# Performance work log

Measured on AMD Instinct MI355X. Metric: run time of the kernel, lower is better.

The kernel has to match this reference:

```python
import jax, jax.numpy as jnp
import numpy as np

B, S, D_MODEL, H = 4, 2048, 1024, 16
HD = D_MODEL // H  # head dim = 64


def setup_inputs() -> dict:
    key = jax.random.key(0)
    k1, k2, k3, k4 = jax.random.split(key, 4)
    x = jax.random.normal(k1, (B, S, D_MODEL), dtype=jnp.float32)
    # weights stored as [d_in, d_out] so projection is x @ W
    scale = 1.0 / np.sqrt(D_MODEL)
    Wq = jax.random.normal(k2, (D_MODEL, D_MODEL), dtype=jnp.float32) * scale
    Wk = jax.random.normal(k3, (D_MODEL, D_MODEL), dtype=jnp.float32) * scale
    Wv = jax.random.normal(k4, (D_MODEL, D_MODEL), dtype=jnp.float32) * scale
    return {"x": x, "Wq": Wq, "Wk": Wk, "Wv": Wv}


def reference(x, Wq, Wk, Wv):
    b, s, d_in = x.shape
    h, hd = H, HD
    # project and split heads -> [b, h, s, hd]
    q = (x @ Wq).reshape(b, s, h, hd).transpose(0, 2, 1, 3)
    k = (x @ Wk).reshape(b, s, h, hd).transpose(0, 2, 1, 3)
    v = (x @ Wv).reshape(b, s, h, hd).transpose(0, 2, 1, 3)
    # raw scores [b, h, s, s]; causal mask (strict upper triangle -> -inf)
    scores = jnp.einsum("bhqd,bhkd->bhqk", q, k)
    causal = jnp.tril(jnp.ones((s, s), dtype=bool))
    scores = jnp.where(causal, scores, -jnp.inf)
    attn = jax.nn.softmax(scores / jnp.sqrt(jnp.float32(hd)), axis=-1)
    ctx = jnp.einsum("bhqk,bhkd->bhqd", attn, v)
    return ctx.transpose(0, 2, 1, 3).reshape(b, s, h * hd)
```

## Files before the change

kernel.cpp:

```cpp
#include <hip/hip_runtime.h>

typedef unsigned short u16;
typedef unsigned int u32;
typedef __bf16 bf16_t;
typedef bf16_t bf16x8 __attribute__((ext_vector_type(8)));
typedef bf16_t bf16x4_t __attribute__((ext_vector_type(4)));
typedef float f32x4 __attribute__((ext_vector_type(4)));
typedef unsigned short ushort8_t __attribute__((ext_vector_type(8)));

#define S_LEN 2048
#define DM 1024
#define NH 16
#define HDIM 64
#define TSTR 136

__device__ __forceinline__ u16 f2b(float f) {
  u32 u = __builtin_bit_cast(u32, f);
  u32 r = (u + 0x7FFFu + ((u >> 16) & 1u)) >> 16;
  return (u16)r;
}

__device__ __forceinline__ void gload16(const void* g, void* l) {
  __builtin_amdgcn_global_load_lds((const __attribute__((address_space(1))) void*)g,
                                   (__attribute__((address_space(3))) void*)l,
                                   16, 0, 0);
}

__device__ __forceinline__ bf16x8 ld_bf8(const u16* p) {
  return *reinterpret_cast<const bf16x8*>(p);
}

__device__ __forceinline__ void stage_rows64(const u16* __restrict__ base, int stride,
                                             u16* __restrict__ dst, int tid, int nchunk) {
#pragma unroll
  for (int i = 0; i < 4; ++i) {
    if (i < nchunk) {
      int ci = i * 256 + tid;
      int row = ci >> 3, col = ci & 7;
      gload16(base + (size_t)row * stride + ((col ^ (row & 7)) << 3), dst + ci * 8);
    }
  }
}
__device__ __forceinline__ void stage_tile256(const u16* __restrict__ base, int stride,
                                              u16* __restrict__ dst, int tid) {
  stage_rows64(base, stride, dst, tid, 2);
}
__device__ __forceinline__ bf16x8 ld_swz64(const u16* lds, int row, int chunk) {
  return ld_bf8(lds + row * 64 + ((chunk ^ (row & 7)) << 3));
}

__global__ __launch_bounds__(256) void k_cvt(const float* __restrict__ in, u16* __restrict__ out) {
  int i = (blockIdx.x * 256 + threadIdx.x) * 4;
  float4 v = *reinterpret_cast<const float4*>(in + i);
  ushort4 o = make_ushort4(f2b(v.x), f2b(v.y), f2b(v.z), f2b(v.w));
  *reinterpret_cast<ushort4*>(out + i) = o;
}

__global__ __launch_bounds__(256) void k_wt3(const float* __restrict__ Wq, const float* __restrict__ Wk,
                                             const float* __restrict__ Wv, u16* __restrict__ Wt) {
  __shared__ float t[32][33];
  const float* W = (blockIdx.z == 0) ? Wq : (blockIdx.z == 1) ? Wk : Wv;
  u16* dst = Wt + (size_t)blockIdx.z * (DM * DM);
  int n0 = blockIdx.x * 32, k0 = blockIdx.y * 32;
  int tx = threadIdx.x & 31, ty = threadIdx.x >> 5;
#pragma unroll
  for (int i = 0; i < 32; i += 8)
    t[ty + i][tx] = W[(size_t)(k0 + ty + i) * DM + n0 + tx];
  __syncthreads();
#pragma unroll
  for (int i = 0; i < 32; i += 8)
    dst[(size_t)(n0 + ty + i) * DM + k0 + tx] = f2b(t[tx][ty + i]);
}

template <bool TRANSPOSED>
__device__ __forceinline__ void gemm_loop(const u16* __restrict__ Ag, const u16* __restrict__ Bg,
                                          u16* __restrict__ At, u16* __restrict__ Bt,
                                          f32x4 (&acc)[4][4], int tid, int l15, int lg,
                                          int wm, int wn) {
  for (int kt = 0; kt < 16; ++kt) {
    int kk = kt * 64;
    stage_rows64(Ag + kk, DM, At, tid, 4);
    stage_rows64(Bg + kk, DM, Bt, tid, 4);
    __syncthreads();
#pragma unroll
    for (int ks = 0; ks < 2; ++ks) {
      bf16x8 af[4], bfr[4];
#pragma unroll
      for (int mi = 0; mi < 4; ++mi)
        af[mi] = ld_swz64(At, wm * 64 + mi * 16 + l15, ks * 4 + lg);
#pragma unroll
      for (int ni = 0; ni < 4; ++ni)
        bfr[ni] = ld_swz64(Bt, wn * 64 + ni * 16 + l15, ks * 4 + lg);
#pragma unroll
      for (int mi = 0; mi < 4; ++mi)
#pragma unroll
        for (int ni = 0; ni < 4; ++ni) {
          if (TRANSPOSED)
            acc[mi][ni] = __builtin_amdgcn_mfma_f32_16x16x32_bf16(bfr[ni], af[mi], acc[mi][ni], 0, 0, 0);
          else
            acc[mi][ni] = __builtin_amdgcn_mfma_f32_16x16x32_bf16(af[mi], bfr[ni], acc[mi][ni], 0, 0, 0);
        }
    }
    __syncthreads();
  }
}

__global__ __launch_bounds__(256, 3) void k_gemm(const u16* __restrict__ Xb, const u16* __restrict__ Wt_all,
                                                 u16* __restrict__ Out_all, u16* __restrict__ Vt,
                                                 float qscale) {
  __shared__ __attribute__((aligned(16))) u16 smem[128 * TSTR];
  u16* At = smem;
  u16* Bt = smem + 8192;
  int bx = blockIdx.x, by = blockIdx.y;
  int n0g = bx * 128, m0 = by * 128;
  int which = n0g >> 10;
  int n0 = n0g & 1023;
  int tid = threadIdx.x;
  int lane = tid & 63, w = tid >> 6;
  int l15 = lane & 15, lg = lane >> 4;
  int wm = w >> 1, wn = w & 1;

  const u16* Ag = Xb + (size_t)m0 * DM;
  const u16* Bg = Wt_all + (size_t)n0g * DM;

  f32x4 acc[4][4] = {};
  u16* T = smem;
  int b = m0 >> 11, s0 = m0 & 2047;
  int base_h = n0 >> 6;

  if (which < 2) {
    gemm_loop<true>(Ag, Bg, At, Bt, acc, tid, l15, lg, wm, wn);
    float scale = (which == 0) ? qscale : 1.0f;
    u16* Out = Out_all + (size_t)which * (size_t)(4 * NH * S_LEN * HDIM);
#pragma unroll
    for (int mi = 0; mi < 4; ++mi) {
#pragma unroll
      for (int ni = 0; ni < 4; ++ni) {
        ushort4 w4 = make_ushort4(f2b(acc[mi][ni][0] * scale), f2b(acc[mi][ni][1] * scale),
                                  f2b(acc[mi][ni][2] * scale), f2b(acc[mi][ni][3] * scale));
        *reinterpret_cast<ushort4*>(T + (wm * 64 + mi * 16 + l15) * TSTR +
                                    wn * 64 + ni * 16 + lg * 4) = w4;
      }
    }
    __syncthreads();
#pragma unroll
    for (int pass = 0; pass < 8; ++pass) {
      int row = pass * 16 + (tid >> 4);
      int col = (tid & 15) * 8;
      ushort8_t v = *reinterpret_cast<const ushort8_t*>(T + row * TSTR + col);
      int h = base_h + (col >> 6), hd = col & 63;
      *reinterpret_cast<ushort8_t*>(Out + ((size_t)(b * NH + h) * S_LEN + s0 + row) * HDIM + hd) = v;
    }
  } else {
    gemm_loop<false>(Ag, Bg, At, Bt, acc, tid, l15, lg, wm, wn);
#pragma unroll
    for (int mi = 0; mi < 4; ++mi) {
#pragma unroll
      for (int ni = 0; ni < 4; ++ni) {
        ushort4 w4 = make_ushort4(f2b(acc[mi][ni][0]), f2b(acc[mi][ni][1]),
                                  f2b(acc[mi][ni][2]), f2b(acc[mi][ni][3]));
        *reinterpret_cast<ushort4*>(T + (wn * 64 + ni * 16 + l15) * TSTR +
                                    wm * 64 + mi * 16 + lg * 4) = w4;
      }
    }
    __syncthreads();
#pragma unroll
    for (int pass = 0; pass < 8; ++pass) {
      int row = pass * 16 + (tid >> 4);
      int col = (tid & 15) * 8;
      ushort8_t v = *reinterpret_cast<const ushort8_t*>(T + row * TSTR + col);
      int h = base_h + (row >> 6), hd = row & 63;
      *reinterpret_cast<ushort8_t*>(Vt + ((size_t)((b * NH + h) * HDIM + hd)) * S_LEN + s0 + col) = v;
    }
  }
}

__device__ __forceinline__ void attn_strip(const u16* __restrict__ Qp, const u16* __restrict__ Kp,
                                           const u16* __restrict__ Vp, float* __restrict__ out,
                                           int b, int h, int qbase, int w, int tid, int lane, int nt,
                                           u16 (*Kd)[64 * 64], u16 (*Vd)[64 * 64],
                                           u16* __restrict__ Pw) {
  int l15 = lane & 15, lg = lane >> 4;
  int qrow = qbase + w * 16;
  bf16x8 qf0 = ld_bf8(Qp + (size_t)(qrow + l15) * HDIM + lg * 8);
  bf16x8 qf1 = ld_bf8(Qp + (size_t)(qrow + l15) * HDIM + 32 + lg * 8);
  f32x4 o[4] = {};
  float ls = 0.f;
  int qa = qrow + l15;
  int psw = (l15 & 7) << 3;

  stage_tile256(Kp, HDIM, Kd[0], tid);
  stage_tile256(Vp, S_LEN, Vd[0], tid);

  for (int kt = 0; kt < nt; ++kt) {
    int k0 = kt * 64;
    int cur = kt & 1;
    asm volatile("s_waitcnt vmcnt(0)" ::: "memory");
    __builtin_amdgcn_sched_barrier(0);
    __builtin_amdgcn_s_barrier();
    __builtin_amdgcn_sched_barrier(0);
    if (kt + 1 < nt) {
      stage_tile256(Kp + (size_t)(k0 + 64) * HDIM, HDIM, Kd[cur ^ 1], tid);
      stage_tile256(Vp + k0 + 64, S_LEN, Vd[cur ^ 1], tid);
    }

    f32x4 sc[4];
    __builtin_amdgcn_s_setprio(1);
#pragma unroll
    for (int kb = 0; kb < 4; ++kb) {
      bf16x8 kf0 = ld_swz64(Kd[cur], kb * 16 + l15, lg);
      bf16x8 kf1 = ld_swz64(Kd[cur], kb * 16 + l15, 4 + lg);
      f32x4 z = {};
      z = __builtin_amdgcn_mfma_f32_16x16x32_bf16(kf0, qf0, z, 0, 0, 0);
      sc[kb] = __builtin_amdgcn_mfma_f32_16x16x32_bf16(kf1, qf1, sc[kb] = z, 0, 0, 0);
    }
    __builtin_amdgcn_s_setprio(0);

    if (kt == nt - 1) {
#pragma unroll
      for (int kb = 0; kb < 4; ++kb) {
        bf16x4_t pw;
#pragma unroll
        for (int r = 0; r < 4; ++r) {
          int key = k0 + kb * 16 + lg * 4 + r;
          float e = __builtin_amdgcn_exp2f(sc[kb][r]);
          e = (key > qa) ? 0.f : e;
          ls += e;
          pw[r] = (bf16_t)e;
        }
        *reinterpret_cast<bf16x4_t*>(Pw + l15 * 64 + ((kb * 16 + lg * 4) ^ psw)) = pw;
      }
    } else {
#pragma unroll
      for (int kb = 0; kb < 4; ++kb) {
        bf16x4_t pw;
#pragma unroll
        for (int r = 0; r < 4; ++r) {
          float e = __builtin_amdgcn_exp2f(sc[kb][r]);
          ls += e;
          pw[r] = (bf16_t)e;
        }
        *reinterpret_cast<bf16x4_t*>(Pw + l15 * 64 + ((kb * 16 + lg * 4) ^ psw)) = pw;
      }
    }
    asm volatile("" ::: "memory");
    bf16x8 pf0 = ld_bf8(Pw + l15 * 64 + ((lg * 8) ^ psw));
    bf16x8 pf1 = ld_bf8(Pw + l15 * 64 + ((32 + lg * 8) ^ psw));

    __builtin_amdgcn_s_setprio(1);
#pragma unroll
    for (int n = 0; n < 4; ++n) {
      bf16x8 vf0 = ld_swz64(Vd[cur], n * 16 + l15, lg);
      bf16x8 vf1 = ld_swz64(Vd[cur], n * 16 + l15, 4 + lg);
      o[n] = __builtin_amdgcn_mfma_f32_16x16x32_bf16(pf0, vf0, o[n], 0, 0, 0);
      o[n] = __builtin_amdgcn_mfma_f32_16x16x32_bf16(pf1, vf1, o[n], 0, 0, 0);
    }
    __builtin_amdgcn_s_setprio(0);
  }

  ls += __shfl_xor(ls, 16);
  ls += __shfl_xor(ls, 32);
  float l0 = __shfl(ls, lg * 4 + 0);
  float l1 = __shfl(ls, lg * 4 + 1);
  float l2 = __shfl(ls, lg * 4 + 2);
  float l3 = __shfl(ls, lg * 4 + 3);
  float lsr[4] = {l0, l1, l2, l3};
#pragma unroll
  for (int r = 0; r < 4; ++r) {
    float inv = 1.f / lsr[r];
    int row = qrow + lg * 4 + r;
#pragma unroll
    for (int n = 0; n < 4; ++n)
      out[((size_t)b * S_LEN + row) * DM + h * HDIM + n * 16 + l15] = o[n][r] * inv;
  }
}

__global__ __launch_bounds__(256, 4) void k_attn(const u16* __restrict__ Qb, const u16* __restrict__ Kb,
                                                 const u16* __restrict__ Vtb, float* __restrict__ out) {
  __shared__ u16 Kd[2][64 * 64];
  __shared__ u16 Vd[2][64 * 64];
  __shared__ u16 Plds[4][16 * 64];
  int j = blockIdx.x;
  int m = j >> 3;
  int x = m & 15;
  int bh = (j & 7) + 8 * (m >> 4);
  int tid = threadIdx.x, lane = tid & 63, w = tid >> 6;
  int b = bh >> 4, h = bh & 15;
  const u16* Qp = Qb + (size_t)bh * S_LEN * HDIM;
  const u16* Kp = Kb + (size_t)bh * S_LEN * HDIM;
  const u16* Vp = Vtb + (size_t)bh * HDIM * S_LEN;
  u16* Pw = Plds[w];
  attn_strip(Qp, Kp, Vp, out, b, h, x * 64, w, tid, lane, x + 1, Kd, Vd, Pw);
  attn_strip(Qp, Kp, Vp, out, b, h, (31 - x) * 64, w, tid, lane, 32 - x, Kd, Vd, Pw);
}

extern "C" void kernel_launch(void* const* d_in, const int* in_sizes, int n_in,
                              void* d_out, int out_size, void* d_ws, size_t ws_size,
                              hipStream_t stream) {
  const float* x  = (const float*)d_in[0];
  const float* Wq = (const float*)d_in[1];
  const float* Wk = (const float*)d_in[2];
  const float* Wv = (const float*)d_in[3];
  float* out = (float*)d_out;

  u16* ws  = (u16*)d_ws;
  u16* xb  = ws;
  u16* wqt = xb + 8388608;
  u16* Qb  = wqt + 3145728;
  u16* Kb  = Qb + 8388608;
  u16* Vtb = Kb + 8388608;

  const float qscale = 0.125f * 1.44269504088896f;

  k_cvt<<<8192, 256, 0, stream>>>(x, xb);
  k_wt3<<<dim3(32, 32, 3), 256, 0, stream>>>(Wq, Wk, Wv, wqt);
  k_gemm<<<dim3(24, 64), 256, 0, stream>>>(xb, wqt, Qb, Vtb, qscale);
  k_attn<<<1024, 256, 0, stream>>>(Qb, Kb, Vtb, out);
}
```

Baseline: 126.9 us.

## Fuse paired causal strips into one K/V sweep sharing staged tiles

The two query strips a block handles (x and 31-x) used to make separate passes over K/V. They now share one loop over the longer strip's key tiles, and the short strip is processed on the same staged tiles while kt <= x. This halves the global-to-LDS K/V staging and removes the second prologue and pipeline ramp. Block-to-x mapping is also reversed for odd groups of 256 to vary scheduling. The cost is more live registers (two sets of Q fragments and accumulators) under launch_bounds(256,4), which risks spills or lower occupancy.

```diff
diff --git a/kernel.cpp b/kernel.cpp
--- a/kernel.cpp
+++ b/kernel.cpp
@@ -175,19 +175,111 @@
   }
 }
 
-__device__ __forceinline__ void attn_strip(const u16* __restrict__ Qp, const u16* __restrict__ Kp,
-                                           const u16* __restrict__ Vp, float* __restrict__ out,
-                                           int b, int h, int qbase, int w, int tid, int lane, int nt,
-                                           u16 (*Kd)[64 * 64], u16 (*Vd)[64 * 64],
-                                           u16* __restrict__ Pw) {
+__device__ __forceinline__ void strip_tile(bool diag, int k0, int qa,
+                                           const u16* __restrict__ Kt, const u16* __restrict__ Vt,
+                                           u16* __restrict__ Pw, int l15, int lg, int psw,
+                                           bf16x8 qf0, bf16x8 qf1, f32x4 (&o)[4], float& ls) {
+  f32x4 sc[4];
+  __builtin_amdgcn_s_setprio(1);
+#pragma unroll
+  for (int kb = 0; kb < 4; ++kb) {
+    bf16x8 kf0 = ld_swz64(Kt, kb * 16 + l15, lg);
+    bf16x8 kf1 = ld_swz64(Kt, kb * 16 + l15, 4 + lg);
+    f32x4 z = {};
+    z = __builtin_amdgcn_mfma_f32_16x16x32_bf16(kf0, qf0, z, 0, 0, 0);
+    sc[kb] = __builtin_amdgcn_mfma_f32_16x16x32_bf16(kf1, qf1, sc[kb] = z, 0, 0, 0);
+  }
+  __builtin_amdgcn_s_setprio(0);
+
+  if (diag) {
+#pragma unroll
+    for (int kb = 0; kb < 4; ++kb) {
+      bf16x4_t pw;
+#pragma unroll
+      for (int r = 0; r < 4; ++r) {
+        int key = k0 + kb * 16 + lg * 4 + r;
+        float e = __builtin_amdgcn_exp2f(sc[kb][r]);
+        e = (key > qa) ? 0.f : e;
+        ls += e;
+        pw[r] = (bf16_t)e;
+      }
+      *reinterpret_cast<bf16x4_t*>(Pw + l15 * 64 + ((kb * 16 + lg * 4) ^ psw)) = pw;
+    }
+  } else {
+#pragma unroll
+    for (int kb = 0; kb < 4; ++kb) {
+      bf16x4_t pw;
+#pragma unroll
+      for (int r = 0; r < 4; ++r) {
+        float e = __builtin_amdgcn_exp2f(sc[kb][r]);
+        ls += e;
+        pw[r] = (bf16_t)e;
+      }
+      *reinterpret_cast<bf16x4_t*>(Pw + l15 * 64 + ((kb * 16 + lg * 4) ^ psw)) = pw;
+    }
+  }
+  asm volatile("" ::: "memory");
+  bf16x8 pf0 = ld_bf8(Pw + l15 * 64 + ((lg * 8) ^ psw));
+  bf16x8 pf1 = ld_bf8(Pw + l15 * 64 + ((32 + lg * 8) ^ psw));
+
+  __builtin_amdgcn_s_setprio(1);
+#pragma unroll
+  for (int n = 0; n < 4; ++n) {
+    bf16x8 vf0 = ld_swz64(Vt, n * 16 + l15, lg);
+    bf16x8 vf1 = ld_swz64(Vt, n * 16 + l15, 4 + lg);
+    o[n] = __builtin_amdgcn_mfma_f32_16x16x32_bf16(pf0, vf0, o[n], 0, 0, 0);
+    o[n] = __builtin_amdgcn_mfma_f32_16x16x32_bf16(pf1, vf1, o[n], 0, 0, 0);
+  }
+  __builtin_amdgcn_s_setprio(0);
+}
+
+__device__ __forceinline__ void strip_out(float* __restrict__ out, int b, int h, int qrow,
+                                          int l15, int lg, f32x4 (&o)[4], float ls) {
+  ls += __shfl_xor(ls, 16);
+  ls += __shfl_xor(ls, 32);
+  float lsr[4];
+#pragma unroll
+  for (int r = 0; r < 4; ++r) lsr[r] = __shfl(ls, lg * 4 + r);
+#pragma unroll
+  for (int r = 0; r < 4; ++r) {
+    float inv = 1.f / lsr[r];
+    int row = qrow + lg * 4 + r;
+#pragma unroll
+    for (int n = 0; n < 4; ++n)
+      out[((size_t)b * S_LEN + row) * DM + h * HDIM + n * 16 + l15] = o[n][r] * inv;
+  }
+}
+
+__global__ __launch_bounds__(256, 4) void k_attn(const u16* __restrict__ Qb, const u16* __restrict__ Kb,
+                                                 const u16* __restrict__ Vtb, float* __restrict__ out) {
+  __shared__ u16 Kd[2][64 * 64];
+  __shared__ u16 Vd[2][64 * 64];
+  __shared__ u16 Plds[4][16 * 64];
+  int j = blockIdx.x;
+  int m = j >> 3;
+  int xr = m & 15;
+  int x = ((j >> 8) & 1) ? (15 - xr) : xr;
+  int bh = (j & 7) + 8 * (m >> 4);
+  int tid = threadIdx.x, lane = tid & 63, w = tid >> 6;
+  int b = bh >> 4, h = bh & 15;
   int l15 = lane & 15, lg = lane >> 4;
-  int qrow = qbase + w * 16;
-  bf16x8 qf0 = ld_bf8(Qp + (size_t)(qrow + l15) * HDIM + lg * 8);
-  bf16x8 qf1 = ld_bf8(Qp + (size_t)(qrow + l15) * HDIM + 32 + lg * 8);
-  f32x4 o[4] = {};
-  float ls = 0.f;
-  int qa = qrow + l15;
   int psw = (l15 & 7) << 3;
+  const u16* Qp = Qb + (size_t)bh * S_LEN * HDIM;
+  const u16* Kp = Kb + (size_t)bh * S_LEN * HDIM;
+  const u16* Vp = Vtb + (size_t)bh * HDIM * S_LEN;
+  u16* Pw = Plds[w];
+
+  int qrowA = x * 64 + w * 16;
+  int qrowB = (31 - x) * 64 + w * 16;
+  int qaA = qrowA + l15, qaB = qrowB + l15;
+  bf16x8 qfA0 = ld_bf8(Qp + (size_t)(qrowA + l15) * HDIM + lg * 8);
+  bf16x8 qfA1 = ld_bf8(Qp + (size_t)(qrowA + l15) * HDIM + 32 + lg * 8);
+  bf16x8 qfB0 = ld_bf8(Qp + (size_t)(qrowB + l15) * HDIM + lg * 8);
+  bf16x8 qfB1 = ld_bf8(Qp + (size_t)(qrowB + l15) * HDIM + 32 + lg * 8);
+  f32x4 oA[4] = {}, oB[4] = {};
+  float lsA = 0.f, lsB = 0.f;
+
+  int nt = 32 - x;
 
   stage_tile256(Kp, HDIM, Kd[0], tid);
   stage_tile256(Vp, S_LEN, Vd[0], tid);
@@ -203,95 +295,13 @@
       stage_tile256(Kp + (size_t)(k0 + 64) * HDIM, HDIM, Kd[cur ^ 1], tid);
       stage_tile256(Vp + k0 + 64, S_LEN, Vd[cur ^ 1], tid);
     }
-
-    f32x4 sc[4];
-    __builtin_amdgcn_s_setprio(1);
-#pragma unroll
-    for (int kb = 0; kb < 4; ++kb) {
-      bf16x8 kf0 = ld_swz64(Kd[cur], kb * 16 + l15, lg);
-      bf16x8 kf1 = ld_swz64(Kd[cur], kb * 16 + l15, 4 + lg);
-      f32x4 z = {};
-      z = __builtin_amdgcn_mfma_f32_16x16x32_bf16(kf0, qf0, z, 0, 0, 0);
-      sc[kb] = __builtin_amdgcn_mfma_f32_16x16x32_bf16(kf1, qf1, sc[kb] = z, 0, 0, 0);
-    }
-    __builtin_amdgcn_s_setprio(0);
-
-    if (kt == nt - 1) {
-#pragma unroll
-      for (int kb = 0; kb < 4; ++kb) {
-        bf16x4_t pw;
-#pragma unroll
-        for (int r = 0; r < 4; ++r) {
-          int key = k0 + kb * 16 + lg * 4 + r;
-          float e = __builtin_amdgcn_exp2f(sc[kb][r]);
-          e = (key > qa) ? 0.f : e;
-          ls += e;
-          pw[r] = (bf16_t)e;
-        }
-        *reinterpret_cast<bf16x4_t*>(Pw + l15 * 64 + ((kb * 16 + lg * 4) ^ psw)) = pw;
-      }
-    } else {
-#pragma unroll
-      for (int kb = 0; kb < 4; ++kb) {
-        bf16x4_t pw;
-#pragma unroll
-        for (int r = 0; r < 4; ++r) {
-          float e = __builtin_amdgcn_exp2f(sc[kb][r]);
-          ls += e;
-          pw[r] = (bf16_t)e;
-        }
-        *reinterpret_cast<bf16x4_t*>(Pw + l15 * 64 + ((kb * 16 + lg * 4) ^ psw)) = pw;
-      }
-    }
-    asm volatile("" ::: "memory");
-    bf16x8 pf0 = ld_bf8(Pw + l15 * 64 + ((lg * 8) ^ psw));
-    bf16x8 pf1 = ld_bf8(Pw + l15 * 64 + ((32 + lg * 8) ^ psw));
-
-    __builtin_amdgcn_s_setprio(1);
-#pragma unroll
-    for (int n = 0; n < 4; ++n) {
-      bf16x8 vf0 = ld_swz64(Vd[cur], n * 16 + l15, lg);
-      bf16x8 vf1 = ld_swz64(Vd[cur], n * 16 + l15, 4 + lg);
-      o[n] = __builtin_amdgcn_mfma_f32_16x16x32_bf16(pf0, vf0, o[n], 0, 0, 0);
-      o[n] = __builtin_amdgcn_mfma_f32_16x16x32_bf16(pf1, vf1, o[n], 0, 0, 0);
-    }
-    __builtin_amdgcn_s_setprio(0);
-  }
-
-  ls += __shfl_xor(ls, 16);
-  ls += __shfl_xor(ls, 32);
-  float l0 = __shfl(ls, lg * 4 + 0);
-  float l1 = __shfl(ls, lg * 4 + 1);
-  float l2 = __shfl(ls, lg * 4 + 2);
-  float l3 = __shfl(ls, lg * 4 + 3);
-  float lsr[4] = {l0, l1, l2, l3};
-#pragma unroll
-  for (int r = 0; r < 4; ++r) {
-    float inv = 1.f / lsr[r];
-    int row = qrow + lg * 4 + r;
-#pragma unroll
-    for (int n = 0; n < 4; ++n)
-      out[((size_t)b * S_LEN + row) * DM + h * HDIM + n * 16 + l15] = o[n][r] * inv;
-  }
-}
-
-__global__ __launch_bounds__(256, 4) void k_attn(const u16* __restrict__ Qb, const u16* __restrict__ Kb,
-                                                 const u16* __restrict__ Vtb, float* __restrict__ out) {
-  __shared__ u16 Kd[2][64 * 64];
-  __shared__ u16 Vd[2][64 * 64];
-  __shared__ u16 Plds[4][16 * 64];
-  int j = blockIdx.x;
-  int m = j >> 3;
-  int x = m & 15;
-  int bh = (j & 7) + 8 * (m >> 4);
-  int tid = threadIdx.x, lane = tid & 63, w = tid >> 6;
-  int b = bh >> 4, h = bh & 15;
-  const u16* Qp = Qb + (size_t)bh * S_LEN * HDIM;
-  const u16* Kp = Kb + (size_t)bh * S_LEN * HDIM;
-  const u16* Vp = Vtb + (size_t)bh * HDIM * S_LEN;
-  u16* Pw = Plds[w];
-  attn_strip(Qp, Kp, Vp, out, b, h, x * 64, w, tid, lane, x + 1, Kd, Vd, Pw);
-  attn_strip(Qp, Kp, Vp, out, b, h, (31 - x) * 64, w, tid, lane, 32 - x, Kd, Vd, Pw);
+    strip_tile(kt == nt - 1, k0, qaB, Kd[cur], Vd[cur], Pw, l15, lg, psw, qfB0, qfB1, oB, lsB);
+    if (kt <= x)
+      strip_tile(kt == x, k0, qaA, Kd[cur], Vd[cur], Pw, l15, lg, psw, qfA0, qfA1, oA, lsA);
+  }
+
+  strip_out(out, b, h, qrowA, l15, lg, oA, lsA);
+  strip_out(out, b, h, qrowB, l15, lg, oB, lsB);
 }
 
 extern "C" void kernel_launch(void* const* d_in, const int* in_sizes, int n_in,
```

Result: no change. 128.1 us (+1.0%).

## Use 32x32 MFMA with 128-row query strips per attention block

Applied to the files above, without the earlier changes.

Reworks the attention kernel so each wave handles 32 query rows with 32x32x16 bf16 MFMAs instead of 16 rows with 16x16x32. Each block now covers 128 query rows, so every staged K/V tile is reused across twice as many queries, and the grid is halved to 512 blocks with paired causal strips. Causal masking now covers the last two key tiles. The larger accumulators and P buffer raise register and LDS use, so launch bounds drop from 4 to 3 blocks per CU, which may hurt latency hiding. Fewer blocks could also leave the GPU less well balanced.

```diff
diff --git a/kernel.cpp b/kernel.cpp
--- a/kernel.cpp
+++ b/kernel.cpp
@@ -6,6 +6,7 @@
 typedef bf16_t bf16x8 __attribute__((ext_vector_type(8)));
 typedef bf16_t bf16x4_t __attribute__((ext_vector_type(4)));
 typedef float f32x4 __attribute__((ext_vector_type(4)));
+typedef float f32x16 __attribute__((ext_vector_type(16)));
 typedef unsigned short ushort8_t __attribute__((ext_vector_type(8)));
 
 #define S_LEN 2048
@@ -175,19 +176,23 @@
   }
 }
 
-__device__ __forceinline__ void attn_strip(const u16* __restrict__ Qp, const u16* __restrict__ Kp,
-                                           const u16* __restrict__ Vp, float* __restrict__ out,
-                                           int b, int h, int qbase, int w, int tid, int lane, int nt,
-                                           u16 (*Kd)[64 * 64], u16 (*Vd)[64 * 64],
-                                           u16* __restrict__ Pw) {
-  int l15 = lane & 15, lg = lane >> 4;
-  int qrow = qbase + w * 16;
-  bf16x8 qf0 = ld_bf8(Qp + (size_t)(qrow + l15) * HDIM + lg * 8);
-  bf16x8 qf1 = ld_bf8(Qp + (size_t)(qrow + l15) * HDIM + 32 + lg * 8);
-  f32x4 o[4] = {};
+__device__ __forceinline__ void attn_strip32(const u16* __restrict__ Qp, const u16* __restrict__ Kp,
+                                             const u16* __restrict__ Vp, float* __restrict__ out,
+                                             int b, int h, int qbase, int w, int tid, int lane, int nt,
+                                             u16 (*Kd)[64 * 64], u16 (*Vd)[64 * 64],
+                                             u16* __restrict__ Pw) {
+  int q = lane & 31, hh = lane >> 5;
+  int qrow = qbase + w * 32;
+  int qa = qrow + q;
+  int psw = (q & 7) << 3;
+
+  bf16x8 qf[4];
+#pragma unroll
+  for (int kc = 0; kc < 4; ++kc)
+    qf[kc] = ld_bf8(Qp + (size_t)(qrow + q) * HDIM + kc * 16 + hh * 8);
+
+  f32x16 o0 = {}, o1 = {};
   float ls = 0.f;
-  int qa = qrow + l15;
-  int psw = (l15 & 7) << 3;
 
   stage_tile256(Kp, HDIM, Kd[0], tid);
   stage_tile256(Vp, S_LEN, Vd[0], tid);
@@ -204,94 +209,82 @@
       stage_tile256(Vp + k0 + 64, S_LEN, Vd[cur ^ 1], tid);
     }
 
-    f32x4 sc[4];
+    f32x16 sc0 = {}, sc1 = {};
     __builtin_amdgcn_s_setprio(1);
 #pragma unroll
-    for (int kb = 0; kb < 4; ++kb) {
-      bf16x8 kf0 = ld_swz64(Kd[cur], kb * 16 + l15, lg);
-      bf16x8 kf1 = ld_swz64(Kd[cur], kb * 16 + l15, 4 + lg);
-      f32x4 z = {};
-      z = __builtin_amdgcn_mfma_f32_16x16x32_bf16(kf0, qf0, z, 0, 0, 0);
-      sc[kb] = __builtin_amdgcn_mfma_f32_16x16x32_bf16(kf1, qf1, sc[kb] = z, 0, 0, 0);
+    for (int kc = 0; kc < 4; ++kc) {
+      bf16x8 kf0 = ld_swz64(Kd[cur], q, 2 * kc + hh);
+      bf16x8 kf1 = ld_swz64(Kd[cur], 32 + q, 2 * kc + hh);
+      sc0 = __builtin_amdgcn_mfma_f32_32x32x16_bf16(kf0, qf[kc], sc0, 0, 0, 0);
+      sc1 = __builtin_amdgcn_mfma_f32_32x32x16_bf16(kf1, qf[kc], sc1, 0, 0, 0);
     }
     __builtin_amdgcn_s_setprio(0);
 
-    if (kt == nt - 1) {
-#pragma unroll
-      for (int kb = 0; kb < 4; ++kb) {
+    bool diag = (kt >= nt - 2);
+#pragma unroll
+    for (int kb = 0; kb < 2; ++kb) {
+#pragma unroll
+      for (int g = 0; g < 4; ++g) {
         bf16x4_t pw;
 #pragma unroll
-        for (int r = 0; r < 4; ++r) {
-          int key = k0 + kb * 16 + lg * 4 + r;
-          float e = __builtin_amdgcn_exp2f(sc[kb][r]);
-          e = (key > qa) ? 0.f : e;
+        for (int rr = 0; rr < 4; ++rr) {
+          float s = (kb == 0) ? sc0[4 * g + rr] : sc1[4 * g + rr];
+          float e = __builtin_amdgcn_exp2f(s);
+          if (diag) {
+            int key = k0 + 32 * kb + 8 * g + 4 * hh + rr;
+            e = (key > qa) ? 0.f : e;
+          }
           ls += e;
-          pw[r] = (bf16_t)e;
+          pw[rr] = (bf16_t)e;
         }
-        *reinterpret_cast<bf16x4_t*>(Pw + l15 * 64 + ((kb * 16 + lg * 4) ^ psw)) = pw;
+        *reinterpret_cast<bf16x4_t*>(Pw + q * 64 + ((32 * kb + 8 * g + 4 * hh) ^ psw)) = pw;
       }
-    } else {
-#pragma unroll
-      for (int kb = 0; kb < 4; ++kb) {
-        bf16x4_t pw;
-#pragma unroll
-        for (int r = 0; r < 4; ++r) {
-          float e = __builtin_amdgcn_exp2f(sc[kb][r]);
-          ls += e;
-          pw[r] = (bf16_t)e;
-        }
-        *reinterpret_cast<bf16x4_t*>(Pw + l15 * 64 + ((kb * 16 + lg * 4) ^ psw)) = pw;
-      }
     }
     asm volatile("" ::: "memory");
-    bf16x8 pf0 = ld_bf8(Pw + l15 * 64 + ((lg * 8) ^ psw));
-    bf16x8 pf1 = ld_bf8(Pw + l15 * 64 + ((32 + lg * 8) ^ psw));
+    bf16x8 pf[4];
+#pragma unroll
+    for (int c = 0; c < 4; ++c)
+      pf[c] = ld_bf8(Pw + q * 64 + ((16 * c + 8 * hh) ^ psw));
 
     __builtin_amdgcn_s_setprio(1);
 #pragma unroll
-    for (int n = 0; n < 4; ++n) {
-      bf16x8 vf0 = ld_swz64(Vd[cur], n * 16 + l15, lg);
-      bf16x8 vf1 = ld_swz64(Vd[cur], n * 16 + l15, 4 + lg);
-      o[n] = __builtin_amdgcn_mfma_f32_16x16x32_bf16(pf0, vf0, o[n], 0, 0, 0);
-      o[n] = __builtin_amdgcn_mfma_f32_16x16x32_bf16(pf1, vf1, o[n], 0, 0, 0);
+    for (int kc = 0; kc < 4; ++kc) {
+      bf16x8 vf0 = ld_swz64(Vd[cur], q, 2 * kc + hh);
+      bf16x8 vf1 = ld_swz64(Vd[cur], 32 + q, 2 * kc + hh);
+      o0 = __builtin_amdgcn_mfma_f32_32x32x16_bf16(pf[kc], vf0, o0, 0, 0, 0);
+      o1 = __builtin_amdgcn_mfma_f32_32x32x16_bf16(pf[kc], vf1, o1, 0, 0, 0);
     }
     __builtin_amdgcn_s_setprio(0);
   }
 
-  ls += __shfl_xor(ls, 16);
   ls += __shfl_xor(ls, 32);
-  float l0 = __shfl(ls, lg * 4 + 0);
-  float l1 = __shfl(ls, lg * 4 + 1);
-  float l2 = __shfl(ls, lg * 4 + 2);
-  float l3 = __shfl(ls, lg * 4 + 3);
-  float lsr[4] = {l0, l1, l2, l3};
-#pragma unroll
-  for (int r = 0; r < 4; ++r) {
-    float inv = 1.f / lsr[r];
-    int row = qrow + lg * 4 + r;
-#pragma unroll
-    for (int n = 0; n < 4; ++n)
-      out[((size_t)b * S_LEN + row) * DM + h * HDIM + n * 16 + l15] = o[n][r] * inv;
-  }
-}
-
-__global__ __launch_bounds__(256, 4) void k_attn(const u16* __restrict__ Qb, const u16* __restrict__ Kb,
+#pragma unroll
+  for (int r = 0; r < 16; ++r) {
+    int qr = (r & 3) + 8 * (r >> 2) + 4 * hh;
+    float inv = 1.f / __shfl(ls, qr);
+    size_t base = ((size_t)b * S_LEN + qrow + qr) * DM + h * HDIM;
+    out[base + q] = o0[r] * inv;
+    out[base + 32 + q] = o1[r] * inv;
+  }
+}
+
+__global__ __launch_bounds__(256, 3) void k_attn(const u16* __restrict__ Qb, const u16* __restrict__ Kb,
                                                  const u16* __restrict__ Vtb, float* __restrict__ out) {
   __shared__ u16 Kd[2][64 * 64];
   __shared__ u16 Vd[2][64 * 64];
-  __shared__ u16 Plds[4][16 * 64];
+  __shared__ u16 Plds[4][32 * 64];
   int j = blockIdx.x;
-  int m = j >> 3;
-  int x = m & 15;
-  int bh = (j & 7) + 8 * (m >> 4);
+  int y = (j >> 3) & 7;
+  int bh = (j & 7) + 8 * (j >> 6);
   int tid = threadIdx.x, lane = tid & 63, w = tid >> 6;
   int b = bh >> 4, h = bh & 15;
   const u16* Qp = Qb + (size_t)bh * S_LEN * HDIM;
   const u16* Kp = Kb + (size_t)bh * S_LEN * HDIM;
   const u16* Vp = Vtb + (size_t)bh * HDIM * S_LEN;
   u16* Pw = Plds[w];
-  attn_strip(Qp, Kp, Vp, out, b, h, x * 64, w, tid, lane, x + 1, Kd, Vd, Pw);
-  attn_strip(Qp, Kp, Vp, out, b, h, (31 - x) * 64, w, tid, lane, 32 - x, Kd, Vd, Pw);
+  attn_strip32(Qp, Kp, Vp, out, b, h, y * 128, w, tid, lane, 2 * y + 2, Kd, Vd, Pw);
+  __syncthreads();
+  attn_strip32(Qp, Kp, Vp, out, b, h, (15 - y) * 128, w, tid, lane, 32 - 2 * y, Kd, Vd, Pw);
 }
 
 extern "C" void kernel_launch(void* const* d_in, const int* in_sizes, int n_in,
@@ -315,5 +308,5 @@
   k_cvt<<<8192, 256, 0, stream>>>(x, xb);
   k_wt3<<<dim3(32, 32, 3), 256, 0, stream>>>(Wq, Wk, Wv, wqt);
   k_gemm<<<dim3(24, 64), 256, 0, stream>>>(xb, wqt, Qb, Vtb, qscale);
-  k_attn<<<1024, 256, 0, stream>>>(Qb, Kb, Vtb, out);
-}
+  k_attn<<<512, 256, 0, stream>>>(Qb, Kb, Vtb, out);
+}
```

Measured after the change: 140.3 us. 10.6% more time.
